# Performance work log

Hardware: AMD Instinct MI355X
Metric: run time of the kernel (lower is better)

The kernel has to match this reference:

```python
import jax, jax.numpy as jnp
import numpy as np

BS, NF, NT = 64, 18, 1500
HID = 256
LH = HID // 2          # lstm hidden dim = 128
T, NC = 6, 2           # 6 detector layers, 2 coords per layer
POS_FEATS = HID // 4   # 64


def lstm_layer(x_seq, W_ih, W_hh, b_ih, b_hh):
    """x_seq: [T, B, D] -> (all hidden states [T, B, H], final hidden [B, H]).
    PyTorch gate order: input, forget, cell(g), output."""
    B = x_seq.shape[1]
    H = W_hh.shape[1]
    h0 = jnp.zeros((B, H), x_seq.dtype)

    def step(carry, x_t):
        h, c = carry
        gates = x_t @ W_ih.T + h @ W_hh.T + (b_ih + b_hh)
        i, f, g, o = jnp.split(gates, 4, axis=-1)
        c = jax.nn.sigmoid(f) * c + jax.nn.sigmoid(i) * jnp.tanh(g)
        h = jax.nn.sigmoid(o) * jnp.tanh(c)
        return (h, c), h

    (hT, _), hs = jax.lax.scan(step, (h0, h0), x_seq)
    return hs, hT


def build_pos_embed_from_eta_phi(deta, dphi, num_feats):
    """DETR-style sine/cosine embedding; output [..., 2*num_feats]."""
    scale = 2.0 * np.pi
    temperature = 10000.0
    dim_t = temperature ** (2.0 * (jnp.arange(num_feats) // 2).astype(jnp.float32) / num_feats)

    def enc(x):
        p = x[..., None] * scale / dim_t                        # [..., num_feats]
        out = jnp.stack([jnp.sin(p[..., 0::2]), jnp.cos(p[..., 1::2])], axis=-1)
        return out.reshape(*p.shape[:-1], num_feats)

    return jnp.concatenate([enc(deta), enc(dphi)], axis=-1)


def setup_inputs() -> dict:
    key = jax.random.key(0)
    ks = jax.random.split(key, 16)
    s = 0.05
    inp = {
        "track_feats": jax.random.normal(ks[0], (BS, NF, NT), dtype=jnp.float32),
        # LSTM layer 0 (input size 2)
        "W_ih0": jax.random.normal(ks[1], (4 * LH, NC), dtype=jnp.float32) * s,
        "W_hh0": jax.random.normal(ks[2], (4 * LH, LH), dtype=jnp.float32) * s,
        "b_ih0": jax.random.normal(ks[3], (4 * LH,), dtype=jnp.float32) * s,
        "b_hh0": jax.random.normal(ks[4], (4 * LH,), dtype=jnp.float32) * s,
        # LSTM layer 1 (input size LH)
        "W_ih1": jax.random.normal(ks[5], (4 * LH, LH), dtype=jnp.float32) * s,
        "W_hh1": jax.random.normal(ks[6], (4 * LH, LH), dtype=jnp.float32) * s,
        "b_ih1": jax.random.normal(ks[7], (4 * LH,), dtype=jnp.float32) * s,
        "b_hh1": jax.random.normal(ks[8], (4 * LH,), dtype=jnp.float32) * s,
        # MLP: (3 + LH) -> HID -> HID, ReLU between
        "mlp_w0": jax.random.normal(ks[9], (HID, 3 + LH), dtype=jnp.float32) * s,
        "mlp_b0": jnp.zeros((HID,), dtype=jnp.float32),
        "mlp_w1": jax.random.normal(ks[10], (HID, HID), dtype=jnp.float32) * s,
        "mlp_b1": jnp.zeros((HID,), dtype=jnp.float32),
    }
    return inp


def reference(track_feats, W_ih0, W_hh0, b_ih0, b_hh0, W_ih1, W_hh1, b_ih1, b_hh1,
              mlp_w0, mlp_b0, mlp_w1, mlp_b1):
    tf = jnp.transpose(track_feats, (0, 2, 1))      # [bs, n_track, 18]
    bs, n_track, _ = tf.shape
    eta = tf[..., 3]
    phi = tf[..., 4]
    logpt = tf[..., 2]

    traj = tf[..., 6:6 + T * NC].reshape(bs * n_track, T, NC)
    x_seq = jnp.transpose(traj, (1, 0, 2))           # [T, bs*n_track, 2]
    hs0, _ = lstm_layer(x_seq, W_ih0, W_hh0, b_ih0, b_hh0)
    _, hT1 = lstm_layer(hs0, W_ih1, W_hh1, b_ih1, b_hh1)
    traj_emb = hT1.reshape(bs, n_track, LH)

    combined = jnp.concatenate([tf[..., 0:3], traj_emb], axis=-1)  # [bs, nt, 3+LH]
    h = jax.nn.relu(combined @ mlp_w0.T + mlp_b0)
    final_embedding = h @ mlp_w1.T + mlp_b1          # [bs, nt, HID]

    pos_encoding = build_pos_embed_from_eta_phi(eta, phi, POS_FEATS)  # [bs, nt, HID//2]
    return (final_embedding, pos_encoding, logpt, eta, phi)
```

## Files before the change

kernel.cpp:

```cpp
#include <hip/hip_runtime.h>
#include <math.h>

#define NTRK   1500
#define BSZ    64
#define NTOT   (NTRK*BSZ)
#define LHID   128
#define TSTEPS 6
#define HID    256

#define TPB    256
#define TPBM   1024
#define MTRK   64
#define NBLK   (NTOT/MTRK)

#define WHH0_OFF 0
#define WIH1_OFF 65536
#define WHH1_OFF 131072
#define W0B_OFF  196608
#define W1B_OFF  229376
#define BX_OFF   294912
#define WS_SHORTS 299008

#define OUT1_OFF ((size_t)NTOT*HID)
#define OUT2_OFF (OUT1_OFF + (size_t)NTOT*(HID/2))
#define OUT3_OFF (OUT2_OFF + (size_t)NTOT)
#define OUT4_OFF (OUT3_OFF + (size_t)NTOT)

typedef __bf16 bf16x8 __attribute__((ext_vector_type(8)));
typedef float  f32x4  __attribute__((ext_vector_type(4)));
typedef float  f32x2  __attribute__((ext_vector_type(2)));

__device__ __forceinline__ unsigned short f2b(float f) {
    union { float f; unsigned u; } v; v.f = f;
    return (unsigned short)((v.u + 0x7FFF + ((v.u >> 16) & 1)) >> 16);
}
__device__ __forceinline__ float sigf(float x) { return 1.0f / (1.0f + __expf(-x)); }
__device__ __forceinline__ float tanhfast(float x) {
    float e = __expf(2.0f * x);
    return (e - 1.0f) / (e + 1.0f);
}

__global__ __launch_bounds__(TPB)
void prep_kernel(const float* __restrict__ Whh0, const float* __restrict__ Wih1,
                 const float* __restrict__ Whh1, const float* __restrict__ w0,
                 const float* __restrict__ w1,  const float* __restrict__ Wih0,
                 const float* __restrict__ bih0, const float* __restrict__ bhh0,
                 unsigned short* __restrict__ ws)
{
    int i = blockIdx.x * TPB + threadIdx.x;
    if (i < 65536)            ws[WHH0_OFF + i] = f2b(Whh0[i]);
    else if (i < 131072)      ws[WIH1_OFF + (i - 65536)]  = f2b(Wih1[i - 65536]);
    else if (i < 196608)      ws[WHH1_OFF + (i - 131072)] = f2b(Whh1[i - 131072]);
    else if (i < 229376) { int j = i - 196608; int n = j >> 7, k = j & 127;
                           ws[W0B_OFF + j] = f2b(w0[n * 131 + 3 + k]); }
    else if (i < 294912)      ws[W1B_OFF + (i - 229376)]  = f2b(w1[i - 229376]);
    else if (i < WS_SHORTS) { int j = i - 294912; int n = j >> 3, k = j & 7;
                              float v = (k == 0) ? Wih0[2 * n]
                                      : (k == 1) ? Wih0[2 * n + 1]
                                      : (k == 2) ? (bih0[n] + bhh0[n]) : 0.0f;
                              ws[BX_OFF + j] = f2b(v); }
}

__device__ __forceinline__ int aoff4(int m, int k) {
    return (((m >> 4) * 4 + (k >> 5)) * 64 + ((k >> 3) & 3) * 16 + (m & 15)) * 8 + (k & 7);
}
__device__ __forceinline__ int aoff8(int m, int k) {
    return (((m >> 4) * 8 + (k >> 5)) * 64 + ((k >> 3) & 3) * 16 + (m & 15)) * 8 + (k & 7);
}

template<int TI>
__device__ __forceinline__ void accumT(f32x4 (&acc)[4][TI],
                                       const unsigned short* __restrict__ Wb,
                                       const unsigned short* hA,
                                       const int (&rowb)[TI], int lane, int quad)
{
    #pragma unroll
    for (int kk = 0; kk < 4; ++kk) {
        bf16x8 a[4];
        #pragma unroll
        for (int mt = 0; mt < 4; ++mt)
            a[mt] = *(const bf16x8*)&hA[((mt * 4 + kk) * 64 + lane) * 8];
        #pragma unroll
        for (int ti = 0; ti < TI; ++ti) {
            bf16x8 b = *(const bf16x8*)&Wb[(size_t)rowb[ti] * 128 + kk * 32 + quad * 8];
            #pragma unroll
            for (int mt = 0; mt < 4; ++mt)
                acc[mt][ti] = __builtin_amdgcn_mfma_f32_16x16x32_bf16(a[mt], b, acc[mt][ti], 0, 0, 0);
        }
    }
}

__global__ __launch_bounds__(TPBM, 4)
void lstm_mlp_mfma(const float* __restrict__ tfeat,
                   const float* __restrict__ bih1, const float* __restrict__ bhh1,
                   const float* __restrict__ w0,  const float* __restrict__ b0,
                   const float* __restrict__ b1,
                   const unsigned short* __restrict__ wsb,
                   float* __restrict__ out)
{
    __shared__ __align__(16) char smem[70144];
    unsigned short* hA0 = (unsigned short*)smem;
    unsigned short* hA1 = (unsigned short*)(smem + 16384);
    float*          pbuf = (float*)(smem + 32768);
    unsigned short* mhA  = (unsigned short*)(smem + 32768);
    unsigned short* xbh  = (unsigned short*)(smem + 66560);
    float (*f5)[8]  = (float(*)[8])(smem + 68096);
    float* outb = (float*)smem;

    const int tid  = threadIdx.x;
    const int w    = tid >> 6;
    const int half = w >> 3;
    const int wl   = w & 7;
    const int lane = tid & 63;
    const int col  = lane & 15;
    const int quad = lane >> 4;
    const int base = blockIdx.x * MTRK;

    if (tid < MTRK * 12) {
        int tl = tid & 63, f = tid >> 6;
        int n = base + tl, b = n / NTRK, tt = n - b * NTRK;
        xbh[tl * 12 + f] = f2b(tfeat[(size_t)(b * 18 + 6 + f) * NTRK + tt]);
    }
    if (tid < MTRK * 5) {
        int tl = tid & 63, f = tid >> 6;
        int n = base + tl, b = n / NTRK, tt = n - b * NTRK;
        f5[tl][f] = tfeat[(size_t)(b * 18 + f) * NTRK + tt];
    }
    __syncthreads();

    const unsigned short* Whh0b = wsb + WHH0_OFF;
    const unsigned short* Wih1b = wsb + WIH1_OFF;
    const unsigned short* Whh1b = wsb + WHH1_OFF;
    const unsigned short* w0b   = wsb + W0B_OFF;
    const unsigned short* w1b   = wsb + W1B_OFF;
    const unsigned short* Bx    = wsb + BX_OFF;

    const int rowp[2] = { half * 128 + wl * 16 + col,
                          256 + half * 128 + wl * 16 + col };
    const float bs1p[2] = { bih1[rowp[0]] + bhh1[rowp[0]],
                            bih1[rowp[1]] + bhh1[rowp[1]] };

    f32x4 c0[4], c1[4];
    #pragma unroll
    for (int mt = 0; mt < 4; ++mt)
        #pragma unroll
        for (int r = 0; r < 4; ++r) { c0[mt][r] = 0.0f; c1[mt][r] = 0.0f; }

    const int u = wl * 16 + col;

    for (int t = 0; t < TSTEPS; ++t) {
        {
            f32x4 acc[4][2];
            {
                bf16x8 ax[4];
                #pragma unroll
                for (int mt = 0; mt < 4; ++mt) {
                    bf16x8 a;
                    #pragma unroll
                    for (int j = 0; j < 8; ++j) a[j] = (__bf16)0.0f;
                    if (quad == 0) {
                        int m = mt * 16 + col;
                        a[0] = *(const __bf16*)&xbh[m * 12 + 2 * t];
                        a[1] = *(const __bf16*)&xbh[m * 12 + 2 * t + 1];
                        a[2] = (__bf16)1.0f;
                    }
                    ax[mt] = a;
                }
                #pragma unroll
                for (int ti = 0; ti < 2; ++ti) {
                    bf16x8 bx;
                    #pragma unroll
                    for (int j = 0; j < 8; ++j) bx[j] = (__bf16)0.0f;
                    if (quad == 0) bx = *(const bf16x8*)&Bx[rowp[ti] * 8];
                    #pragma unroll
                    for (int mt = 0; mt < 4; ++mt) {
                        f32x4 z = {0.0f, 0.0f, 0.0f, 0.0f};
                        acc[mt][ti] = __builtin_amdgcn_mfma_f32_16x16x32_bf16(ax[mt], bx, z, 0, 0, 0);
                    }
                }
            }
            if (t > 0) accumT<2>(acc, Whh0b, hA0, rowp, lane, quad);
            if (half == 0) {
                #pragma unroll
                for (int mt = 0; mt < 4; ++mt)
                    #pragma unroll
                    for (int r = 0; r < 4; ++r)
                        pbuf[(mt * 16 + quad * 4 + r) * 132 + u] =
                            sigf(acc[mt][0][r]) * tanhfast(acc[mt][1][r]);
            }
            __syncthreads();
            if (half == 1) {
                #pragma unroll
                for (int mt = 0; mt < 4; ++mt)
                    #pragma unroll
                    for (int r = 0; r < 4; ++r) {
                        int m = mt * 16 + quad * 4 + r;
                        float p  = pbuf[m * 132 + u];
                        float cn = sigf(acc[mt][0][r]) * c0[mt][r] + p;
                        c0[mt][r] = cn;
                        hA0[aoff4(m, u)] = f2b(sigf(acc[mt][1][r]) * tanhfast(cn));
                    }
            }
            __syncthreads();
        }

        {
            f32x4 acc[4][2];
            #pragma unroll
            for (int mt = 0; mt < 4; ++mt)
                #pragma unroll
                for (int r = 0; r < 4; ++r) {
                    acc[mt][0][r] = bs1p[0];
                    acc[mt][1][r] = bs1p[1];
                }
            accumT<2>(acc, Wih1b, hA0, rowp, lane, quad);
            if (t > 0) accumT<2>(acc, Whh1b, hA1, rowp, lane, quad);
            if (half == 0) {
                #pragma unroll
                for (int mt = 0; mt < 4; ++mt)
                    #pragma unroll
                    for (int r = 0; r < 4; ++r)
                        pbuf[(mt * 16 + quad * 4 + r) * 132 + u] =
                            sigf(acc[mt][0][r]) * tanhfast(acc[mt][1][r]);
            }
            __syncthreads();
            if (half == 1) {
                #pragma unroll
                for (int mt = 0; mt < 4; ++mt)
                    #pragma unroll
                    for (int r = 0; r < 4; ++r) {
                        int m = mt * 16 + quad * 4 + r;
                        float p  = pbuf[m * 132 + u];
                        float cn = sigf(acc[mt][0][r]) * c1[mt][r] + p;
                        c1[mt][r] = cn;
                        hA1[aoff4(m, u)] = f2b(sigf(acc[mt][1][r]) * tanhfast(cn));
                    }
            }
            __syncthreads();
        }
    }

    const int rowm = w * 16 + col;
    {
        f32x4 am[4][1];
        {
            float bm  = b0[rowm];
            float wf0 = w0[rowm * 131 + 0], wf1 = w0[rowm * 131 + 1], wf2 = w0[rowm * 131 + 2];
            #pragma unroll
            for (int mt = 0; mt < 4; ++mt)
                #pragma unroll
                for (int r = 0; r < 4; ++r) {
                    int m = mt * 16 + quad * 4 + r;
                    am[mt][0][r] = bm + f5[m][0] * wf0 + f5[m][1] * wf1 + f5[m][2] * wf2;
                }
        }
        const int rowa[1] = { rowm };
        accumT<1>(am, w0b, hA1, rowa, lane, quad);
        #pragma unroll
        for (int mt = 0; mt < 4; ++mt)
            #pragma unroll
            for (int r = 0; r < 4; ++r) {
                int m = mt * 16 + quad * 4 + r;
                mhA[aoff8(m, rowm)] = f2b(fmaxf(am[mt][0][r], 0.0f));
            }
        __syncthreads();
    }

    {
        f32x4 ao[4];
        {
            float bv = b1[rowm];
            #pragma unroll
            for (int mt = 0; mt < 4; ++mt)
                #pragma unroll
                for (int r = 0; r < 4; ++r) ao[mt][r] = bv;
        }
        #pragma unroll
        for (int kk = 0; kk < 8; ++kk) {
            bf16x8 a[4];
            #pragma unroll
            for (int mt = 0; mt < 4; ++mt)
                a[mt] = *(const bf16x8*)&mhA[((mt * 8 + kk) * 64 + lane) * 8];
            bf16x8 b = *(const bf16x8*)&w1b[(size_t)rowm * 256 + kk * 32 + quad * 8];
            #pragma unroll
            for (int mt = 0; mt < 4; ++mt)
                ao[mt] = __builtin_amdgcn_mfma_f32_16x16x32_bf16(a[mt], b, ao[mt], 0, 0, 0);
        }
        __syncthreads();

        #pragma unroll
        for (int mt = 0; mt < 4; ++mt)
            #pragma unroll
            for (int r = 0; r < 4; ++r)
                outb[(mt * 16 + quad * 4 + r) * 260 + rowm] = ao[mt][r];
        __syncthreads();

        for (int i = tid; i < MTRK * 64; i += TPBM) {
            int row = i >> 6, c4 = (i & 63) << 2;
            f32x4 v = *(const f32x4*)&outb[row * 260 + c4];
            __builtin_nontemporal_store(v, (f32x4*)(out + (size_t)(base + row) * HID + c4));
        }
    }

    {
        const int tl = tid >> 4;
        const int ml = tid & 15;
        const int n  = base + tl;
        const float eta   = f5[tl][3];
        const float phi   = f5[tl][4];
        const float TWO_PI = 6.28318530717958647692f;
        float* o1 = out + OUT1_OFF + (size_t)n * (HID / 2);
        #pragma unroll
        for (int i = 0; i < 2; ++i) {
            int m = ml + i * 16;
            float inv = exp2f(-(float)m * (13.28771237954945f / 32.0f));
            float pe = eta * TWO_PI * inv;
            float pp = phi * TWO_PI * inv;
            f32x2 ve = { sinf(pe), cosf(pe) };
            f32x2 vp = { sinf(pp), cosf(pp) };
            __builtin_nontemporal_store(ve, (f32x2*)(o1 + 2 * m));
            __builtin_nontemporal_store(vp, (f32x2*)(o1 + 64 + 2 * m));
        }
        if (ml == 0) {
            __builtin_nontemporal_store(f5[tl][2], out + OUT2_OFF + n);
            __builtin_nontemporal_store(eta, out + OUT3_OFF + n);
            __builtin_nontemporal_store(phi, out + OUT4_OFF + n);
        }
    }
}

extern "C" void kernel_launch(void* const* d_in, const int* in_sizes, int n_in,
                              void* d_out, int out_size, void* d_ws, size_t ws_size,
                              hipStream_t stream)
{
    const float* tfeat = (const float*)d_in[0];
    const float* Wih0  = (const float*)d_in[1];
    const float* Whh0  = (const float*)d_in[2];
    const float* bih0  = (const float*)d_in[3];
    const float* bhh0  = (const float*)d_in[4];
    const float* Wih1  = (const float*)d_in[5];
    const float* Whh1  = (const float*)d_in[6];
    const float* bih1  = (const float*)d_in[7];
    const float* bhh1  = (const float*)d_in[8];
    const float* w0    = (const float*)d_in[9];
    const float* b0    = (const float*)d_in[10];
    const float* w1    = (const float*)d_in[11];
    const float* b1    = (const float*)d_in[12];
    float* out = (float*)d_out;
    unsigned short* wsb = (unsigned short*)d_ws;

    hipLaunchKernelGGL(prep_kernel, dim3(WS_SHORTS / TPB), dim3(TPB), 0, stream,
                       Whh0, Wih1, Whh1, w0, w1, Wih0, bih0, bhh0, wsb);
    hipLaunchKernelGGL(lstm_mlp_mfma, dim3(NBLK), dim3(TPBM), 0, stream,
                       tfeat, bih1, bhh1, w0, b0, b1, wsb, out);
}
```

Before: 1.089 ms.

## Pipeline LSTM layers across wave groups with double-buffered hidden states

The two LSTM layers were computed one after the other by all 16 waves, with the gate work split between the two halves and exchanged through a shared buffer, costing four barriers per timestep. Now wave group 0 runs layer 0 at step p while wave group 1 runs layer 1 at step p-1. Each wave computes all four gates for its hidden units, so no exchange buffer is needed. Hidden states are double-buffered in LDS, giving one barrier per pipeline stage (7 in total). The trade-off is that each wave does twice the gate MFMA work per step and there is one extra pipeline stage.

```diff
diff --git a/kernel.cpp b/kernel.cpp
--- a/kernel.cpp
+++ b/kernel.cpp
@@ -98,18 +98,19 @@
                    const unsigned short* __restrict__ wsb,
                    float* __restrict__ out)
 {
-    __shared__ __align__(16) char smem[70144];
-    unsigned short* hA0 = (unsigned short*)smem;
-    unsigned short* hA1 = (unsigned short*)(smem + 16384);
-    float*          pbuf = (float*)(smem + 32768);
-    unsigned short* mhA  = (unsigned short*)(smem + 32768);
-    unsigned short* xbh  = (unsigned short*)(smem + 66560);
-    float (*f5)[8]  = (float(*)[8])(smem + 68096);
+    __shared__ __align__(16) char smem[69120];
+    unsigned short* h0_0 = (unsigned short*)smem;
+    unsigned short* h0_1 = (unsigned short*)(smem + 16384);
+    unsigned short* h1_0 = (unsigned short*)(smem + 32768);
+    unsigned short* h1_1 = (unsigned short*)(smem + 49152);
+    unsigned short* mhA  = (unsigned short*)smem;
+    unsigned short* xbh  = (unsigned short*)(smem + 65536);
+    float (*f5)[8]  = (float(*)[8])(smem + 67072);
     float* outb = (float*)smem;
 
     const int tid  = threadIdx.x;
     const int w    = tid >> 6;
-    const int half = w >> 3;
+    const int wgrp = w >> 3;
     const int wl   = w & 7;
     const int lane = tid & 63;
     const int col  = lane & 15;
@@ -135,23 +136,28 @@
     const unsigned short* w1b   = wsb + W1B_OFF;
     const unsigned short* Bx    = wsb + BX_OFF;
 
-    const int rowp[2] = { half * 128 + wl * 16 + col,
-                          256 + half * 128 + wl * 16 + col };
-    const float bs1p[2] = { bih1[rowp[0]] + bhh1[rowp[0]],
-                            bih1[rowp[1]] + bhh1[rowp[1]] };
-
-    f32x4 c0[4], c1[4];
+    const int rows_ig[2] = { 0 * 128 + wl * 16 + col, 2 * 128 + wl * 16 + col };
+    const int rows_fo[2] = { 1 * 128 + wl * 16 + col, 3 * 128 + wl * 16 + col };
+    const float bsig[2] = { bih1[rows_ig[0]] + bhh1[rows_ig[0]],
+                            bih1[rows_ig[1]] + bhh1[rows_ig[1]] };
+    const float bsfo[2] = { bih1[rows_fo[0]] + bhh1[rows_fo[0]],
+                            bih1[rows_fo[1]] + bhh1[rows_fo[1]] };
+
+    f32x4 cst[4];
     #pragma unroll
     for (int mt = 0; mt < 4; ++mt)
         #pragma unroll
-        for (int r = 0; r < 4; ++r) { c0[mt][r] = 0.0f; c1[mt][r] = 0.0f; }
+        for (int r = 0; r < 4; ++r) cst[mt][r] = 0.0f;
 
     const int u = wl * 16 + col;
 
-    for (int t = 0; t < TSTEPS; ++t) {
-        {
-            f32x4 acc[4][2];
-            {
+    for (int p = 0; p < TSTEPS + 1; ++p) {
+        if (wgrp == 0) {
+            if (p < TSTEPS) {
+                const int t = p;
+                unsigned short*       h0w = (t & 1) ? h0_1 : h0_0;
+                const unsigned short* h0r = (t & 1) ? h0_0 : h0_1;
+
                 bf16x8 ax[4];
                 #pragma unroll
                 for (int mt = 0; mt < 4; ++mt) {
@@ -166,79 +172,107 @@
                     }
                     ax[mt] = a;
                 }
-                #pragma unroll
-                for (int ti = 0; ti < 2; ++ti) {
-                    bf16x8 bx;
-                    #pragma unroll
-                    for (int j = 0; j < 8; ++j) bx[j] = (__bf16)0.0f;
-                    if (quad == 0) bx = *(const bf16x8*)&Bx[rowp[ti] * 8];
-                    #pragma unroll
-                    for (int mt = 0; mt < 4; ++mt) {
-                        f32x4 z = {0.0f, 0.0f, 0.0f, 0.0f};
-                        acc[mt][ti] = __builtin_amdgcn_mfma_f32_16x16x32_bf16(ax[mt], bx, z, 0, 0, 0);
+
+                f32x4 pig[4];
+                {
+                    f32x4 acc[4][2];
+                    #pragma unroll
+                    for (int ti = 0; ti < 2; ++ti) {
+                        bf16x8 bx;
+                        #pragma unroll
+                        for (int j = 0; j < 8; ++j) bx[j] = (__bf16)0.0f;
+                        if (quad == 0) bx = *(const bf16x8*)&Bx[rows_ig[ti] * 8];
+                        #pragma unroll
+                        for (int mt = 0; mt < 4; ++mt) {
+                            f32x4 z = {0.0f, 0.0f, 0.0f, 0.0f};
+                            acc[mt][ti] = __builtin_amdgcn_mfma_f32_16x16x32_bf16(ax[mt], bx, z, 0, 0, 0);
+                        }
                     }
+                    if (t > 0) accumT<2>(acc, Whh0b, h0r, rows_ig, lane, quad);
+                    #pragma unroll
+                    for (int mt = 0; mt < 4; ++mt)
+                        #pragma unroll
+                        for (int r = 0; r < 4; ++r)
+                            pig[mt][r] = sigf(acc[mt][0][r]) * tanhfast(acc[mt][1][r]);
+                }
+                {
+                    f32x4 acc[4][2];
+                    #pragma unroll
+                    for (int ti = 0; ti < 2; ++ti) {
+                        bf16x8 bx;
+                        #pragma unroll
+                        for (int j = 0; j < 8; ++j) bx[j] = (__bf16)0.0f;
+                        if (quad == 0) bx = *(const bf16x8*)&Bx[rows_fo[ti] * 8];
+                        #pragma unroll
+                        for (int mt = 0; mt < 4; ++mt) {
+                            f32x4 z = {0.0f, 0.0f, 0.0f, 0.0f};
+                            acc[mt][ti] = __builtin_amdgcn_mfma_f32_16x16x32_bf16(ax[mt], bx, z, 0, 0, 0);
+                        }
+                    }
+                    if (t > 0) accumT<2>(acc, Whh0b, h0r, rows_fo, lane, quad);
+                    #pragma unroll
+                    for (int mt = 0; mt < 4; ++mt)
+                        #pragma unroll
+                        for (int r = 0; r < 4; ++r) {
+                            float cn = sigf(acc[mt][0][r]) * cst[mt][r] + pig[mt][r];
+                            cst[mt][r] = cn;
+                            int m = mt * 16 + quad * 4 + r;
+                            h0w[aoff4(m, u)] = f2b(sigf(acc[mt][1][r]) * tanhfast(cn));
+                        }
                 }
             }
-            if (t > 0) accumT<2>(acc, Whh0b, hA0, rowp, lane, quad);
-            if (half == 0) {
-                #pragma unroll
-                for (int mt = 0; mt < 4; ++mt)
-                    #pragma unroll
-                    for (int r = 0; r < 4; ++r)
-                        pbuf[(mt * 16 + quad * 4 + r) * 132 + u] =
-                            sigf(acc[mt][0][r]) * tanhfast(acc[mt][1][r]);
+        } else {
+            if (p >= 1) {
+                const int s = p - 1;
+                const unsigned short* h0r = (s & 1) ? h0_1 : h0_0;
+                unsigned short*       h1w = (s & 1) ? h1_1 : h1_0;
+                const unsigned short* h1r = (s & 1) ? h1_0 : h1_1;
+
+                f32x4 pig[4];
+                {
+                    f32x4 acc[4][2];
+                    #pragma unroll
+                    for (int mt = 0; mt < 4; ++mt)
+                        #pragma unroll
+                        for (int r = 0; r < 4; ++r) {
+                            acc[mt][0][r] = bsig[0];
+                            acc[mt][1][r] = bsig[1];
+                        }
+                    accumT<2>(acc, Wih1b, h0r, rows_ig, lane, quad);
+                    if (s > 0) accumT<2>(acc, Whh1b, h1r, rows_ig, lane, quad);
+                    #pragma unroll
+                    for (int mt = 0; mt < 4; ++mt)
+                        #pragma unroll
+                        for (int r = 0; r < 4; ++r)
+                            pig[mt][r] = sigf(acc[mt][0][r]) * tanhfast(acc[mt][1][r]);
+                }
+                {
+                    f32x4 acc[4][2];
+                    #pragma unroll
+                    for (int mt = 0; mt < 4; ++mt)
+                        #pragma unroll
+                        for (int r = 0; r < 4; ++r) {
+                            acc[mt][0][r] = bsfo[0];
+                            acc[mt][1][r] = bsfo[1];
+                        }
+                    accumT<2>(acc, Wih1b, h0r, rows_fo, lane, quad);
+                    if (s > 0) accumT<2>(acc, Whh1b, h1r, rows_fo, lane, quad);
+                    #pragma unroll
+                    for (int mt = 0; mt < 4; ++mt)
+                        #pragma unroll
+                        for (int r = 0; r < 4; ++r) {
+                            float cn = sigf(acc[mt][0][r]) * cst[mt][r] + pig[mt][r];
+                            cst[mt][r] = cn;
+                            int m = mt * 16 + quad * 4 + r;
+                            h1w[aoff4(m, u)] = f2b(sigf(acc[mt][1][r]) * tanhfast(cn));
+                        }
+                }
             }
-            __syncthreads();
-            if (half == 1) {
-                #pragma unroll
-                for (int mt = 0; mt < 4; ++mt)
-                    #pragma unroll
-                    for (int r = 0; r < 4; ++r) {
-                        int m = mt * 16 + quad * 4 + r;
-                        float p  = pbuf[m * 132 + u];
-                        float cn = sigf(acc[mt][0][r]) * c0[mt][r] + p;
-                        c0[mt][r] = cn;
-                        hA0[aoff4(m, u)] = f2b(sigf(acc[mt][1][r]) * tanhfast(cn));
-                    }
-            }
-            __syncthreads();
-        }
-
-        {
-            f32x4 acc[4][2];
-            #pragma unroll
-            for (int mt = 0; mt < 4; ++mt)
-                #pragma unroll
-                for (int r = 0; r < 4; ++r) {
-                    acc[mt][0][r] = bs1p[0];
-                    acc[mt][1][r] = bs1p[1];
-                }
-            accumT<2>(acc, Wih1b, hA0, rowp, lane, quad);
-            if (t > 0) accumT<2>(acc, Whh1b, hA1, rowp, lane, quad);
-            if (half == 0) {
-                #pragma unroll
-                for (int mt = 0; mt < 4; ++mt)
-                    #pragma unroll
-                    for (int r = 0; r < 4; ++r)
-                        pbuf[(mt * 16 + quad * 4 + r) * 132 + u] =
-                            sigf(acc[mt][0][r]) * tanhfast(acc[mt][1][r]);
-            }
-            __syncthreads();
-            if (half == 1) {
-                #pragma unroll
-                for (int mt = 0; mt < 4; ++mt)
-                    #pragma unroll
-                    for (int r = 0; r < 4; ++r) {
-                        int m = mt * 16 + quad * 4 + r;
-                        float p  = pbuf[m * 132 + u];
-                        float cn = sigf(acc[mt][0][r]) * c1[mt][r] + p;
-                        c1[mt][r] = cn;
-                        hA1[aoff4(m, u)] = f2b(sigf(acc[mt][1][r]) * tanhfast(cn));
-                    }
-            }
-            __syncthreads();
-        }
-    }
+        }
+        __syncthreads();
+    }
+
+    const unsigned short* h1f = h1_1;
 
     const int rowm = w * 16 + col;
     {
@@ -255,7 +289,7 @@
                 }
         }
         const int rowa[1] = { rowm };
-        accumT<1>(am, w0b, hA1, rowa, lane, quad);
+        accumT<1>(am, w0b, h1f, rowa, lane, quad);
         #pragma unroll
         for (int mt = 0; mt < 4; ++mt)
             #pragma unroll
```

Measured after the change: 1.135 ms. 1.04x slower.
